# Kernel tuning notes

Measured on AMD Instinct MI355X. Metric: run time of the kernel, lower is better.

## Reference

```python
import jax, jax.numpy as jnp
import numpy as np

N_HEADS = 32
N_KV_HEADS = 8
HEAD_DIM = 128
GROUP = N_HEADS // N_KV_HEADS  # 4
MAX_SEQ_LEN = 4096
DIM = 3072
NEG_BIG = 1.0e9


def setup_inputs() -> dict:
    key = jax.random.key(0)
    ks = jax.random.split(key, 8)
    B, T = 1, 2048
    return {
        "x": jax.random.normal(ks[0], (B, T, DIM), dtype=jnp.float32),
        "freqs_cos": jax.random.uniform(ks[1], (T, HEAD_DIM // 2), dtype=jnp.float32),
        "freqs_sin": jax.random.uniform(ks[2], (T, HEAD_DIM // 2), dtype=jnp.float32),
        "input_pos": jnp.arange(T, dtype=jnp.int32),
        "wq": jax.random.normal(ks[3], (N_HEADS * HEAD_DIM, DIM), dtype=jnp.float32) * 0.02,
        "wk": jax.random.normal(ks[4], (N_KV_HEADS * HEAD_DIM, DIM), dtype=jnp.float32) * 0.02,
        "wv": jax.random.normal(ks[5], (N_KV_HEADS * HEAD_DIM, DIM), dtype=jnp.float32) * 0.02,
        "wo": jax.random.normal(ks[6], (DIM, N_HEADS * HEAD_DIM), dtype=jnp.float32) * 0.02,
        "k_cache": jnp.zeros((1, N_KV_HEADS, MAX_SEQ_LEN, HEAD_DIM), dtype=jnp.float32),
        "v_cache": jnp.zeros((1, N_KV_HEADS, MAX_SEQ_LEN, HEAD_DIM), dtype=jnp.float32),
    }


def _rotate_half(x):
    half = x.shape[-1] // 2
    return jnp.concatenate([-x[..., half:], x[..., :half]], axis=-1)


def _apply_rope(q, k, freqs_cos, freqs_sin):
    # freqs: [T, D/2] -> [1, T, 1, D] (tiled x2, matching torch repeat on last dim)
    fc = jnp.concatenate([freqs_cos, freqs_cos], axis=-1)[None, :, None, :]
    fs = jnp.concatenate([freqs_sin, freqs_sin], axis=-1)[None, :, None, :]
    qf = q.astype(jnp.float32)
    kf = k.astype(jnp.float32)
    q_out = qf * fc + _rotate_half(qf) * fs
    k_out = kf * fc + _rotate_half(kf) * fs
    return q_out.astype(q.dtype), k_out.astype(k.dtype)


def reference(x, freqs_cos, freqs_sin, input_pos, wq, wk, wv, wo, k_cache, v_cache):
    B, T, _ = x.shape
    # QKV projections
    q = (x @ wq.T).reshape(B, T, N_HEADS, HEAD_DIM)
    k = (x @ wk.T).reshape(B, T, N_KV_HEADS, HEAD_DIM)
    v = (x @ wv.T).reshape(B, T, N_KV_HEADS, HEAD_DIM)
    # split-half RoPE (computed in fp32)
    q, k = _apply_rope(q, k, freqs_cos, freqs_sin)
    # StaticKVCache.update: scatter [B,H,T,D] into [1,H,S,D] cache at input_pos (dim 2)
    kc = k_cache.at[:, :, input_pos].set(k.transpose(0, 2, 1, 3))
    vc = v_cache.at[:, :, input_pos].set(v.transpose(0, 2, 1, 3))
    # MetalSDPA: additive causal mask over full cache length
    S = kc.shape[2]
    k_pos = jnp.arange(S)
    valid = jnp.clip(input_pos[:, None] - k_pos[None, :] + 1, 0, 1)  # [T, S]
    mask = (valid.astype(q.dtype) - 1.0) * NEG_BIG
    # GQA attention: group q heads per kv head
    qg = q.transpose(0, 2, 1, 3).reshape(B, N_KV_HEADS, GROUP, T, HEAD_DIM)
    scale = 1.0 / jnp.sqrt(jnp.asarray(HEAD_DIM, dtype=q.dtype))
    scores = jnp.einsum('bhgtd,bhsd->bhgts', qg, kc) * scale + mask  # [B,Hk,G,T,S]
    attn = jax.nn.softmax(scores, axis=-1)
    y = jnp.einsum('bhgts,bhsd->bhgtd', attn, vc)
    y = y.reshape(B, N_HEADS, T, HEAD_DIM).transpose(0, 2, 1, 3).reshape(B, T, N_HEADS * HEAD_DIM)
    return y @ wo.T
```

## Files before the change

kernel.cpp:

```cpp
#include <hip/hip_runtime.h>

typedef __attribute__((ext_vector_type(8))) short bf16x8;
typedef __attribute__((ext_vector_type(4))) float f32x4;

#define T_SEQ   2048
#define DIM     3072
#define NQH     32
#define NKVH    8
#define HD      128
#define QDIM    4096
#define KVDIM   1024
#define QKVDIM  6144

#define AS1 __attribute__((address_space(1)))
#define AS3 __attribute__((address_space(3)))

static __device__ __forceinline__ unsigned short f2bf(float f) {
  unsigned u = __float_as_uint(f);
  u += 0x7FFFu + ((u >> 16) & 1u);
  return (unsigned short)(u >> 16);
}
static __device__ __forceinline__ float bf2f(unsigned short h) {
  return __uint_as_float(((unsigned)h) << 16);
}
static __device__ __forceinline__ unsigned pkbf(float lo, float hi) {
  unsigned r;
  asm("v_cvt_pk_bf16_f32 %0, %1, %2" : "=v"(r) : "v"(lo), "v"(hi));
  return r;
}

static __device__ __forceinline__ void gload_lds16(const unsigned short* g, unsigned short* l) {
  __builtin_amdgcn_global_load_lds((AS1 void*)(g), (AS3 void*)(l), 16, 0, 0);
}

__global__ void cvt_f32_bf16(const float* __restrict__ src, unsigned short* __restrict__ dst, int n4) {
  int i = blockIdx.x * blockDim.x + threadIdx.x;
  if (i >= n4) return;
  float4 v = reinterpret_cast<const float4*>(src)[i];
  ushort4 o;
  o.x = f2bf(v.x); o.y = f2bf(v.y); o.z = f2bf(v.z); o.w = f2bf(v.w);
  reinterpret_cast<ushort4*>(dst)[i] = o;
}

template<int OUTBF>
__global__ __launch_bounds__(256) void gemm_bt(
    const unsigned short* __restrict__ A, const unsigned short* __restrict__ B,
    float* __restrict__ Cf, unsigned short* __restrict__ Cb,
    int M, int N, int K) {
  __shared__ unsigned short la[128 * 64];
  __shared__ unsigned short lb[128 * 64];
  const int nbx = N >> 7;
  const int q8 = gridDim.x >> 3;
  int bid = blockIdx.x;
  bid = (bid & 7) * q8 + (bid >> 3);
  const int bx = bid % nbx, by = bid / nbx;
  const int tid = threadIdx.x;
  const int ln = tid & 63;
  const int wave = tid >> 6;
  const int lr = ln & 15, lg = ln >> 4;
  const int wr = wave >> 1, wc = wave & 1;
  const int rowA0 = by << 7, rowB0 = bx << 7;

  f32x4 acc[4][4] = {};

  const int ktn = K >> 6;
  for (int kt = 0; kt < ktn; kt++) {
    __syncthreads();
#pragma unroll
    for (int it = 0; it < 4; it++) {
      int ci = it * 256 + tid;
      int r = ci >> 3, cpos = ci & 7;
      int c = cpos ^ (r & 7);
      const unsigned short* gA = A + (size_t)(rowA0 + r) * K + kt * 64 + c * 8;
      const unsigned short* gB = B + (size_t)(rowB0 + r) * K + kt * 64 + c * 8;
      gload_lds16(gA, &la[ci * 8]);
      gload_lds16(gB, &lb[ci * 8]);
    }
    __syncthreads();
#pragma unroll
    for (int kk = 0; kk < 2; kk++) {
      bf16x8 af[4], bfr[4];
#pragma unroll
      for (int mi = 0; mi < 4; mi++) {
        int r = wr * 64 + mi * 16 + lr;
        int p = (kk * 4 + lg) ^ (r & 7);
        af[mi] = *reinterpret_cast<const bf16x8*>(&la[r * 64 + p * 8]);
      }
#pragma unroll
      for (int ni = 0; ni < 4; ni++) {
        int r = wc * 64 + ni * 16 + lr;
        int p = (kk * 4 + lg) ^ (r & 7);
        bfr[ni] = *reinterpret_cast<const bf16x8*>(&lb[r * 64 + p * 8]);
      }
#pragma unroll
      for (int mi = 0; mi < 4; mi++)
#pragma unroll
        for (int ni = 0; ni < 4; ni++)
          acc[mi][ni] = __builtin_amdgcn_mfma_f32_16x16x32_bf16(af[mi], bfr[ni], acc[mi][ni], 0, 0, 0);
    }
  }
#pragma unroll
  for (int mi = 0; mi < 4; mi++)
#pragma unroll
    for (int ni = 0; ni < 4; ni++)
#pragma unroll
      for (int j = 0; j < 4; j++) {
        int r = rowA0 + wr * 64 + mi * 16 + lg * 4 + j;
        int cc = rowB0 + wc * 64 + ni * 16 + lr;
        if (OUTBF) Cb[(size_t)r * N + cc] = f2bf(acc[mi][ni][j]);
        else       Cf[(size_t)r * N + cc] = acc[mi][ni][j];
      }
}

__global__ void rope_repack(const unsigned short* __restrict__ qkv,
                            const float* __restrict__ fc, const float* __restrict__ fs,
                            unsigned short* __restrict__ qo, unsigned short* __restrict__ ko) {
  int idx = blockIdx.x * blockDim.x + threadIdx.x;
  int d = idx & 63;
  int hh = (idx >> 6) % 40;
  int t = idx / 2560;
  const unsigned short* src = qkv + (size_t)t * QKVDIM + hh * 128;
  float x0 = bf2f(src[d]);
  float x1 = bf2f(src[d + 64]);
  float c = fc[t * 64 + d], s = fs[t * 64 + d];
  float o0 = x0 * c - x1 * s;
  float o1 = x1 * c + x0 * s;
  if (hh < 32) {
    unsigned short* dst = qo + (size_t)t * QDIM + hh * 128;
    dst[d] = f2bf(o0); dst[d + 64] = f2bf(o1);
  } else {
    unsigned short* dst = ko + (size_t)t * KVDIM + (hh - 32) * 128;
    dst[d] = f2bf(o0); dst[d + 64] = f2bf(o1);
  }
}

__global__ void vtrans(const unsigned short* __restrict__ qkv, unsigned short* __restrict__ vt) {
  __shared__ unsigned short tile[64][68];
  int tb = blockIdx.x * 64, cb = blockIdx.y * 64;
  int tid = threadIdx.x;
#pragma unroll
  for (int i = 0; i < 16; i++) {
    int e = i * 256 + tid;
    int tl = e >> 6, cl = e & 63;
    tile[tl][cl] = qkv[(size_t)(tb + tl) * QKVDIM + 5120 + cb + cl];
  }
  __syncthreads();
#pragma unroll
  for (int i = 0; i < 16; i++) {
    int e = i * 256 + tid;
    int cl = e >> 6, tl = e & 63;
    vt[(size_t)(cb + cl) * T_SEQ + tb + tl] = tile[tl][cl];
  }
}

__global__ __launch_bounds__(256) void attn_fwd(
    const unsigned short* __restrict__ q, const unsigned short* __restrict__ k,
    const unsigned short* __restrict__ vt, unsigned short* __restrict__ y) {
  __shared__ unsigned short k_lds[2][32 * 128];
  __shared__ unsigned short v_lds[2][128 * 32];
  __shared__ unsigned short p_lds[4][16 * 40];
  __shared__ float a_lds[4][16];
  const int tid = threadIdx.x;
  const int ln = tid & 63;
  const int wave = tid >> 6;
  const int lr = ln & 15, lg = ln >> 4;

  const int kh = blockIdx.x & 7;
  const int i = blockIdx.x >> 3;
  const int qh = i & 3;
  const int pr = i >> 2;
  const int qta = pr, qtb = 31 - pr;
  const int h = kh * 4 + qh;

  const int qra0 = qta * 64 + wave * 16, qrowa = qra0 + lr;
  const int qrb0 = qtb * 64 + wave * 16, qrowb = qrb0 + lr;
  const float SL2E = 0.08838834764831845f * 1.44269504088896f;
  const float NEGINF = -__builtin_inff();

  bf16x8 qfa[4], qfb[4];
  {
    const unsigned short* qba = q + (size_t)qrowa * QDIM + h * HD + lg * 8;
    const unsigned short* qbb = q + (size_t)qrowb * QDIM + h * HD + lg * 8;
#pragma unroll
    for (int dc = 0; dc < 4; dc++) {
      qfa[dc] = *reinterpret_cast<const bf16x8*>(qba + dc * 32);
      qfb[dc] = *reinterpret_cast<const bf16x8*>(qbb + dc * 32);
    }
  }

  f32x4 acca[8] = {}, accb[8] = {};
  float ma = NEGINF, la = 0.f, mb = NEGINF, lb = 0.f;

  const int krow0 = tid >> 4,  kcol0 = tid & 15;
  const int krow1 = 16 + krow0;
  const int vrow0 = tid >> 2,  vcol0 = tid & 3;
  const int vrow1 = 64 + vrow0;

  auto tile_compute = [&](int sb, int cur, const bf16x8 (&qf)[4], f32x4 (&acc)[8],
                          float& m, float& lsum, int qr0, int qrow) {
    f32x4 s0t = {0.f, 0.f, 0.f, 0.f}, s1t = {0.f, 0.f, 0.f, 0.f};
    __builtin_amdgcn_s_setprio(1);
#pragma unroll
    for (int dc = 0; dc < 4; dc++) {
      int c = lg + dc * 4;
      int p = c ^ (lr & 7);
      bf16x8 a0 = *reinterpret_cast<const bf16x8*>(&k_lds[cur][lr * 128 + p * 8]);
      bf16x8 a1 = *reinterpret_cast<const bf16x8*>(&k_lds[cur][(lr + 16) * 128 + p * 8]);
      s0t = __builtin_amdgcn_mfma_f32_16x16x32_bf16(a0, qf[dc], s0t, 0, 0, 0);
      s1t = __builtin_amdgcn_mfma_f32_16x16x32_bf16(a1, qf[dc], s1t, 0, 0, 0);
    }
    __builtin_amdgcn_s_setprio(0);

    float vv[8];
    if (sb + 31 <= qr0) {
#pragma unroll
      for (int jj = 0; jj < 4; jj++) { vv[jj] = s0t[jj]; vv[jj + 4] = s1t[jj]; }
    } else {
      const int base0 = sb + lg * 4;
#pragma unroll
      for (int jj = 0; jj < 4; jj++) {
        vv[jj]     = (base0 + jj      <= qrow) ? s0t[jj] : NEGINF;
        vv[jj + 4] = (base0 + jj + 16 <= qrow) ? s1t[jj] : NEGINF;
      }
    }

    float mx = fmaxf(fmaxf(fmaxf(vv[0], vv[1]), fmaxf(vv[2], vv[3])),
                     fmaxf(fmaxf(vv[4], vv[5]), fmaxf(vv[6], vv[7])));
    mx = fmaxf(mx, __shfl_xor(mx, 16));
    mx = fmaxf(mx, __shfl_xor(mx, 32));

    const bool doresc = __any(mx > m + 60.0f);
    const float mn = doresc ? fmaxf(m, mx) : m;

    float p[8], ps = 0.f;
#pragma unroll
    for (int ii = 0; ii < 8; ii++) { p[ii] = exp2f((vv[ii] - mn) * SL2E); ps += p[ii]; }
    ps += __shfl_xor(ps, 16);
    ps += __shfl_xor(ps, 32);

    uint2 w0, w1;
    w0.x = pkbf(p[0], p[1]); w0.y = pkbf(p[2], p[3]);
    w1.x = pkbf(p[4], p[5]); w1.y = pkbf(p[6], p[7]);
    *reinterpret_cast<uint2*>(&p_lds[wave][lr * 40 + lg * 4])      = w0;
    *reinterpret_cast<uint2*>(&p_lds[wave][lr * 40 + 16 + lg * 4]) = w1;

    if (doresc) {
      const float alpha = exp2f((m - mn) * SL2E);
      lsum = lsum * alpha + ps;
      m = mn;
      a_lds[wave][lr] = alpha;
      asm volatile("s_waitcnt lgkmcnt(0)" ::: "memory");
      float4 a4 = *reinterpret_cast<const float4*>(&a_lds[wave][lg * 4]);
#pragma unroll
      for (int dc2 = 0; dc2 < 8; dc2++) {
        acc[dc2][0] *= a4.x; acc[dc2][1] *= a4.y;
        acc[dc2][2] *= a4.z; acc[dc2][3] *= a4.w;
      }
    } else {
      lsum += ps;
      asm volatile("s_waitcnt lgkmcnt(0)" ::: "memory");
    }

    bf16x8 pa = *reinterpret_cast<const bf16x8*>(&p_lds[wave][lr * 40 + lg * 8]);
    __builtin_amdgcn_s_setprio(1);
#pragma unroll
    for (int dc2 = 0; dc2 < 8; dc2++) {
      int d = dc2 * 16 + lr;
      int p2 = lg ^ ((d >> 1) & 3);
      bf16x8 bv = *reinterpret_cast<const bf16x8*>(&v_lds[cur][d * 32 + p2 * 8]);
      acc[dc2] = __builtin_amdgcn_mfma_f32_16x16x32_bf16(pa, bv, acc[dc2], 0, 0, 0);
    }
    __builtin_amdgcn_s_setprio(0);
  };

  const int ntiles = (qtb * 64 + 95) >> 5;

  {
    bf16x8 kr0 = *reinterpret_cast<const bf16x8*>(k + (size_t)krow0 * KVDIM + kh * HD + kcol0 * 8);
    bf16x8 kr1 = *reinterpret_cast<const bf16x8*>(k + (size_t)krow1 * KVDIM + kh * HD + kcol0 * 8);
    bf16x8 vr0 = *reinterpret_cast<const bf16x8*>(vt + (size_t)(kh * HD + vrow0) * T_SEQ + vcol0 * 8);
    bf16x8 vr1 = *reinterpret_cast<const bf16x8*>(vt + (size_t)(kh * HD + vrow1) * T_SEQ + vcol0 * 8);
    *reinterpret_cast<bf16x8*>(&k_lds[0][krow0 * 128 + (kcol0 ^ (krow0 & 7)) * 8]) = kr0;
    *reinterpret_cast<bf16x8*>(&k_lds[0][krow1 * 128 + (kcol0 ^ (krow1 & 7)) * 8]) = kr1;
    *reinterpret_cast<bf16x8*>(&v_lds[0][vrow0 * 32 + (vcol0 ^ ((vrow0 >> 1) & 3)) * 8]) = vr0;
    *reinterpret_cast<bf16x8*>(&v_lds[0][vrow1 * 32 + (vcol0 ^ ((vrow1 >> 1) & 3)) * 8]) = vr1;
  }
  __syncthreads();

  for (int st = 0; st < ntiles; st++) {
    const int sb = st * 32;
    const int cur = st & 1;
    const bool more = (st + 1 < ntiles);

    bf16x8 kr0, kr1, vr0, vr1;
    if (more) {
      const int sb1 = sb + 32;
      kr0 = *reinterpret_cast<const bf16x8*>(k + (size_t)(sb1 + krow0) * KVDIM + kh * HD + kcol0 * 8);
      kr1 = *reinterpret_cast<const bf16x8*>(k + (size_t)(sb1 + krow1) * KVDIM + kh * HD + kcol0 * 8);
      vr0 = *reinterpret_cast<const bf16x8*>(vt + (size_t)(kh * HD + vrow0) * T_SEQ + sb1 + vcol0 * 8);
      vr1 = *reinterpret_cast<const bf16x8*>(vt + (size_t)(kh * HD + vrow1) * T_SEQ + sb1 + vcol0 * 8);
    }

    if (sb <= qrb0 + 15) tile_compute(sb, cur, qfb, accb, mb, lb, qrb0, qrowb);
    if (sb <= qra0 + 15) tile_compute(sb, cur, qfa, acca, ma, la, qra0, qrowa);

    if (more) {
      const int nxt = cur ^ 1;
      *reinterpret_cast<bf16x8*>(&k_lds[nxt][krow0 * 128 + (kcol0 ^ (krow0 & 7)) * 8]) = kr0;
      *reinterpret_cast<bf16x8*>(&k_lds[nxt][krow1 * 128 + (kcol0 ^ (krow1 & 7)) * 8]) = kr1;
      *reinterpret_cast<bf16x8*>(&v_lds[nxt][vrow0 * 32 + (vcol0 ^ ((vrow0 >> 1) & 3)) * 8]) = vr0;
      *reinterpret_cast<bf16x8*>(&v_lds[nxt][vrow1 * 32 + (vcol0 ^ ((vrow1 >> 1) & 3)) * 8]) = vr1;
      __syncthreads();
    }
  }

  a_lds[wave][lr] = 1.0f / lb;
  asm volatile("s_waitcnt lgkmcnt(0)" ::: "memory");
  float4 l4 = *reinterpret_cast<const float4*>(&a_lds[wave][lg * 4]);
  {
    float li[4] = {l4.x, l4.y, l4.z, l4.w};
#pragma unroll
    for (int jj = 0; jj < 4; jj++) {
      int r = qrb0 + lg * 4 + jj;
#pragma unroll
      for (int dc2 = 0; dc2 < 8; dc2++)
        y[(size_t)r * QDIM + h * HD + dc2 * 16 + lr] = f2bf(accb[dc2][jj] * li[jj]);
    }
  }
  a_lds[wave][lr] = 1.0f / la;
  asm volatile("s_waitcnt lgkmcnt(0)" ::: "memory");
  l4 = *reinterpret_cast<const float4*>(&a_lds[wave][lg * 4]);
  {
    float li[4] = {l4.x, l4.y, l4.z, l4.w};
#pragma unroll
    for (int jj = 0; jj < 4; jj++) {
      int r = qra0 + lg * 4 + jj;
#pragma unroll
      for (int dc2 = 0; dc2 < 8; dc2++)
        y[(size_t)r * QDIM + h * HD + dc2 * 16 + lr] = f2bf(acca[dc2][jj] * li[jj]);
    }
  }
}

extern "C" void kernel_launch(void* const* d_in, const int* in_sizes, int n_in,
                              void* d_out, int out_size, void* d_ws, size_t ws_size,
                              hipStream_t stream) {
  (void)in_sizes; (void)n_in; (void)out_size; (void)ws_size;
  const float* x    = (const float*)d_in[0];
  const float* fcos = (const float*)d_in[1];
  const float* fsin = (const float*)d_in[2];
  const float* wq   = (const float*)d_in[4];
  const float* wk   = (const float*)d_in[5];
  const float* wv   = (const float*)d_in[6];
  const float* wo   = (const float*)d_in[7];
  float* out = (float*)d_out;
  char* ws = (char*)d_ws;

  unsigned short* x_bf    = (unsigned short*)(ws);
  unsigned short* wqkv_bf = (unsigned short*)(ws + 12582912);
  unsigned short* qkv_bf  = (unsigned short*)(ws + 50331648);
  unsigned short* q_bf    = (unsigned short*)(ws);
  unsigned short* k_bf    = (unsigned short*)(ws + 16777216);
  unsigned short* vt_bf   = (unsigned short*)(ws + 20971520);
  unsigned short* y_bf    = (unsigned short*)(ws + 25165824);
  unsigned short* wo_bf   = (unsigned short*)(ws + 50331648);

  cvt_f32_bf16<<<6144,  256, 0, stream>>>(x,  x_bf,               2048 * 3072 / 4);
  cvt_f32_bf16<<<12288, 256, 0, stream>>>(wq, wqkv_bf,            4096 * 3072 / 4);
  cvt_f32_bf16<<<3072,  256, 0, stream>>>(wk, wqkv_bf + 4096*3072, 1024 * 3072 / 4);
  cvt_f32_bf16<<<3072,  256, 0, stream>>>(wv, wqkv_bf + 5120*3072, 1024 * 3072 / 4);
  gemm_bt<1><<<768, 256, 0, stream>>>(x_bf, wqkv_bf, nullptr, qkv_bf, 2048, 6144, 3072);

  rope_repack<<<20480, 256, 0, stream>>>(qkv_bf, fcos, fsin, q_bf, k_bf);
  vtrans<<<dim3(32, 16), 256, 0, stream>>>(qkv_bf, vt_bf);

  cvt_f32_bf16<<<12288, 256, 0, stream>>>(wo, wo_bf, 3072 * 4096 / 4);
  attn_fwd<<<512, 256, 0, stream>>>(q_bf, k_bf, vt_bf, y_bf);
  gemm_bt<0><<<384, 256, 0, stream>>>(y_bf, wo_bf, out, nullptr, 2048, 3072, 4096);
}
```

Before: 326.5 us.

## Replace GEMM with 256x256-tile, 4-stage pipelined global-to-LDS kernel

Both projection GEMMs now use a 512-thread kernel with a 256x256 output tile and BK=32. A 4-deep ring of LDS buffers is filled ahead by direct global-to-LDS loads, with manual vmcnt/lgkmcnt waits, a single barrier per k-step and MFMA priority boosts. The goal is to hide global load latency and raise arithmetic intensity per block. In exchange the grids shrink to 192 and 96 blocks, which may leave many CUs idle. The new LDS layout also drops the XOR swizzle, so bank conflicts are possible.

```diff
diff --git a/kernel.cpp b/kernel.cpp
--- a/kernel.cpp
+++ b/kernel.cpp
@@ -43,13 +43,13 @@
 }
 
 template<int OUTBF>
-__global__ __launch_bounds__(256) void gemm_bt(
+__global__ __launch_bounds__(512, 2) void gemm256(
     const unsigned short* __restrict__ A, const unsigned short* __restrict__ B,
     float* __restrict__ Cf, unsigned short* __restrict__ Cb,
     int M, int N, int K) {
-  __shared__ unsigned short la[128 * 64];
-  __shared__ unsigned short lb[128 * 64];
-  const int nbx = N >> 7;
+  __shared__ unsigned short ldsA[4][256 * 32];
+  __shared__ unsigned short ldsB[4][256 * 32];
+  const int nbx = N >> 8;
   const int q8 = gridDim.x >> 3;
   int bid = blockIdx.x;
   bid = (bid & 7) * q8 + (bid >> 3);
@@ -58,54 +58,78 @@
   const int ln = tid & 63;
   const int wave = tid >> 6;
   const int lr = ln & 15, lg = ln >> 4;
-  const int wr = wave >> 1, wc = wave & 1;
-  const int rowA0 = by << 7, rowB0 = bx << 7;
-
-  f32x4 acc[4][4] = {};
-
-  const int ktn = K >> 6;
-  for (int kt = 0; kt < ktn; kt++) {
-    __syncthreads();
-#pragma unroll
-    for (int it = 0; it < 4; it++) {
-      int ci = it * 256 + tid;
-      int r = ci >> 3, cpos = ci & 7;
-      int c = cpos ^ (r & 7);
-      const unsigned short* gA = A + (size_t)(rowA0 + r) * K + kt * 64 + c * 8;
-      const unsigned short* gB = B + (size_t)(rowB0 + r) * K + kt * 64 + c * 8;
-      gload_lds16(gA, &la[ci * 8]);
-      gload_lds16(gB, &lb[ci * 8]);
-    }
-    __syncthreads();
-#pragma unroll
-    for (int kk = 0; kk < 2; kk++) {
-      bf16x8 af[4], bfr[4];
-#pragma unroll
-      for (int mi = 0; mi < 4; mi++) {
-        int r = wr * 64 + mi * 16 + lr;
-        int p = (kk * 4 + lg) ^ (r & 7);
-        af[mi] = *reinterpret_cast<const bf16x8*>(&la[r * 64 + p * 8]);
-      }
-#pragma unroll
-      for (int ni = 0; ni < 4; ni++) {
-        int r = wc * 64 + ni * 16 + lr;
-        int p = (kk * 4 + lg) ^ (r & 7);
-        bfr[ni] = *reinterpret_cast<const bf16x8*>(&lb[r * 64 + p * 8]);
-      }
-#pragma unroll
-      for (int mi = 0; mi < 4; mi++)
-#pragma unroll
-        for (int ni = 0; ni < 4; ni++)
-          acc[mi][ni] = __builtin_amdgcn_mfma_f32_16x16x32_bf16(af[mi], bfr[ni], acc[mi][ni], 0, 0, 0);
-    }
-  }
-#pragma unroll
-  for (int mi = 0; mi < 4; mi++)
+  const int wr = wave >> 2, wc = wave & 3;
+  const int rowA0 = by << 8, rowB0 = bx << 8;
+
+  const int ci0 = tid, ci1 = tid + 512;
+  const int r0 = ci0 >> 2, cp0 = ci0 & 3;
+  const int r1 = ci1 >> 2, cp1 = ci1 & 3;
+
+  f32x4 acc[8][4] = {};
+
+  const int ktn = K >> 5;
+
+  auto STAGE = [&](int kt, int bufi) {
+    const unsigned short* Ak = A + (size_t)kt * 32;
+    const unsigned short* Bk = B + (size_t)kt * 32;
+    gload_lds16(Ak + (size_t)(rowA0 + r0) * K + cp0 * 8, &ldsA[bufi][ci0 * 8]);
+    gload_lds16(Ak + (size_t)(rowA0 + r1) * K + cp1 * 8, &ldsA[bufi][ci1 * 8]);
+    gload_lds16(Bk + (size_t)(rowB0 + r0) * K + cp0 * 8, &ldsB[bufi][ci0 * 8]);
+    gload_lds16(Bk + (size_t)(rowB0 + r1) * K + cp1 * 8, &ldsB[bufi][ci1 * 8]);
+  };
+
+  STAGE(0, 0); STAGE(1, 1); STAGE(2, 2);
+  asm volatile("s_waitcnt vmcnt(8)" ::: "memory");
+  __builtin_amdgcn_s_barrier();
+
+  for (int t = 0; t < ktn; t++) {
+    const int c = t & 3;
+    if (t + 3 < ktn) STAGE(t + 3, (t + 3) & 3);
+
+    bf16x8 bf_[4], af_[4];
 #pragma unroll
     for (int ni = 0; ni < 4; ni++)
+      bf_[ni] = *reinterpret_cast<const bf16x8*>(&ldsB[c][(wc * 64 + ni * 16 + lr) * 32 + lg * 8]);
+#pragma unroll
+    for (int mi = 0; mi < 4; mi++)
+      af_[mi] = *reinterpret_cast<const bf16x8*>(&ldsA[c][(wr * 128 + mi * 16 + lr) * 32 + lg * 8]);
+    asm volatile("s_waitcnt lgkmcnt(0)" ::: "memory");
+    __builtin_amdgcn_sched_barrier(0);
+    __builtin_amdgcn_s_setprio(1);
+#pragma unroll
+    for (int mi = 0; mi < 4; mi++)
+#pragma unroll
+      for (int ni = 0; ni < 4; ni++)
+        acc[mi][ni] = __builtin_amdgcn_mfma_f32_16x16x32_bf16(af_[mi], bf_[ni], acc[mi][ni], 0, 0, 0);
+    __builtin_amdgcn_s_setprio(0);
+
+    bf16x8 ag_[4];
+#pragma unroll
+    for (int mi = 0; mi < 4; mi++)
+      ag_[mi] = *reinterpret_cast<const bf16x8*>(&ldsA[c][(wr * 128 + (mi + 4) * 16 + lr) * 32 + lg * 8]);
+    asm volatile("s_waitcnt lgkmcnt(0)" ::: "memory");
+    __builtin_amdgcn_sched_barrier(0);
+    __builtin_amdgcn_s_setprio(1);
+#pragma unroll
+    for (int mi = 0; mi < 4; mi++)
+#pragma unroll
+      for (int ni = 0; ni < 4; ni++)
+        acc[mi + 4][ni] = __builtin_amdgcn_mfma_f32_16x16x32_bf16(ag_[mi], bf_[ni], acc[mi + 4][ni], 0, 0, 0);
+    __builtin_amdgcn_s_setprio(0);
+
+    if (t < ktn - 3)       { asm volatile("s_waitcnt vmcnt(8)" ::: "memory"); }
+    else if (t == ktn - 3) { asm volatile("s_waitcnt vmcnt(4)" ::: "memory"); }
+    else if (t == ktn - 2) { asm volatile("s_waitcnt vmcnt(0)" ::: "memory"); }
+    if (t < ktn - 1) __builtin_amdgcn_s_barrier();
+  }
+
+#pragma unroll
+  for (int mi = 0; mi < 8; mi++)
+#pragma unroll
+    for (int ni = 0; ni < 4; ni++)
 #pragma unroll
       for (int j = 0; j < 4; j++) {
-        int r = rowA0 + wr * 64 + mi * 16 + lg * 4 + j;
+        int r = rowA0 + wr * 128 + mi * 16 + lg * 4 + j;
         int cc = rowB0 + wc * 64 + ni * 16 + lr;
         if (OUTBF) Cb[(size_t)r * N + cc] = f2bf(acc[mi][ni][j]);
         else       Cf[(size_t)r * N + cc] = acc[mi][ni][j];
@@ -369,12 +393,12 @@
   cvt_f32_bf16<<<12288, 256, 0, stream>>>(wq, wqkv_bf,            4096 * 3072 / 4);
   cvt_f32_bf16<<<3072,  256, 0, stream>>>(wk, wqkv_bf + 4096*3072, 1024 * 3072 / 4);
   cvt_f32_bf16<<<3072,  256, 0, stream>>>(wv, wqkv_bf + 5120*3072, 1024 * 3072 / 4);
-  gemm_bt<1><<<768, 256, 0, stream>>>(x_bf, wqkv_bf, nullptr, qkv_bf, 2048, 6144, 3072);
+  gemm256<1><<<192, 512, 0, stream>>>(x_bf, wqkv_bf, nullptr, qkv_bf, 2048, 6144, 3072);
 
   rope_repack<<<20480, 256, 0, stream>>>(qkv_bf, fcos, fsin, q_bf, k_bf);
   vtrans<<<dim3(32, 16), 256, 0, stream>>>(qkv_bf, vt_bf);
 
   cvt_f32_bf16<<<12288, 256, 0, stream>>>(wo, wo_bf, 3072 * 4096 / 4);
   attn_fwd<<<512, 256, 0, stream>>>(q_bf, k_bf, vt_bf, y_bf);
-  gemm_bt<0><<<384, 256, 0, stream>>>(y_bf, wo_bf, out, nullptr, 2048, 3072, 4096);
-}
+  gemm256<0><<<96, 512, 0, stream>>>(y_bf, wo_bf, out, nullptr, 2048, 3072, 4096);
+}
```

After: 429.4 us. +31.5%, slower.
